# Performance work log

Measured on AMD Instinct MI355X. Metric: run time of the kernel, lower is better.

## Reference

```python
import jax, jax.numpy as jnp
import numpy as np

N = 2048
HID = 1024
Z = 256
DIM = 128 + 64 * 3 + 32 * 5  # 480
FAN = 128 * 128 + 64 * 64 + 32 * 32  # total fan-in over all CG paths


def _ln(x, g, b, eps=1e-6):
    mu = jnp.mean(x, axis=-1, keepdims=True)
    var = jnp.mean((x - mu) ** 2, axis=-1, keepdims=True)
    return (x - mu) * jax.lax.rsqrt(var + eps) * g + b


def _fctp(t, w0, w1, w2):
    # FullyConnectedTensorProduct(irreps, irreps, 'HIDx0e'):
    # only l1==l2 -> 0e paths survive; CG is delta_{m1,m2}/sqrt(2l+1).
    x0 = t[:, :128]                       # 128x0e
    x1 = t[:, 128:320].reshape(-1, 64, 3)  # 64x1o
    x2 = t[:, 320:480].reshape(-1, 32, 5)  # 32x2e
    e0 = jnp.einsum('bu,bv,uvh->bh', x0, x0, w0)
    e1 = jnp.einsum('bum,bvm,uvh->bh', x1, x1, w1) / np.sqrt(3.0)
    e2 = jnp.einsum('bum,bvm,uvh->bh', x2, x2, w2) / np.sqrt(5.0)
    return (e0 + e1 + e2) / np.sqrt(float(FAN))  # component normalization


def _head(t, w0, w1, w2, W1, b1, g1, be1, W2, b2, g2, be2):
    h = _fctp(t, w0, w1, w2)
    h = jax.nn.silu(_ln(h @ W1 + b1, g1, be1))
    h = jax.nn.silu(_ln(h @ W2 + b2, g2, be2))
    return h  # [N, Z]


def setup_inputs() -> dict:
    key = jax.random.key(0)
    ks = jax.random.split(key, 6)
    return {
        'tensor_in': jax.random.normal(ks[0], (N, DIM), jnp.float32),
        'w0': jax.random.normal(ks[1], (128, 128, HID), jnp.float32),
        'w1': jax.random.normal(ks[2], (64, 64, HID), jnp.float32),
        'w2': jax.random.normal(ks[3], (32, 32, HID), jnp.float32),
        'W1': jax.random.normal(ks[4], (HID, HID), jnp.float32) / np.sqrt(HID),
        'b1': jnp.zeros((HID,), jnp.float32),
        'g1': jnp.ones((HID,), jnp.float32),
        'be1': jnp.zeros((HID,), jnp.float32),
        'W2': jax.random.normal(ks[5], (HID, Z), jnp.float32) / np.sqrt(HID),
        'b2': jnp.zeros((Z,), jnp.float32),
        'g2': jnp.ones((Z,), jnp.float32),
        'be2': jnp.zeros((Z,), jnp.float32),
    }


def reference(tensor_in, w0, w1, w2, W1, b1, g1, be1, W2, b2, g2, be2):
    f = lambda t: _head(t, w0, w1, w2, W1, b1, g1, be1, W2, b2, g2, be2)
    x, pullback = jax.vjp(f, tensor_in)
    # torch: grad(x, tensor_in, grad_outputs=ones_like(x), create_graph=True)
    y = pullback(jnp.ones_like(x))[0]
    return x, y
```

## Files before the change

kernel.cpp:

```cpp
#include <hip/hip_runtime.h>
#include <math.h>

typedef unsigned short u16;
typedef __bf16 bf16x8 __attribute__((ext_vector_type(8)));
typedef float f32x4 __attribute__((ext_vector_type(4)));

#define NPACK  11264
#define NVALID 10864
#define BASE1  8256
#define BASE2  10336

__device__ __forceinline__ u16 f2bf(float f) {
    unsigned u = __builtin_bit_cast(unsigned, f);
    u += 0x7FFFu + ((u >> 16) & 1u);
    return (u16)(u >> 16);
}
__device__ __forceinline__ float bf2f(u16 h) {
    return __builtin_bit_cast(float, ((unsigned)h) << 16);
}

#define GLOAD_LDS16(g, l)                                                     \
    __builtin_amdgcn_global_load_lds(                                         \
        (const __attribute__((address_space(1))) void*)(g),                   \
        (__attribute__((address_space(3))) void*)(l), 16, 0, 0)

__device__ __forceinline__ int pk0(int a, int b) {
    int u = min(a, b), v = max(a, b);
    return u * 128 - (u * (u - 1)) / 2 + (v - u);
}
__device__ __forceinline__ int pk1(int a, int b) {
    int u = min(a, b), v = max(a, b);
    return BASE1 + u * 64 - (u * (u - 1)) / 2 + (v - u);
}
__device__ __forceinline__ int pk2(int a, int b) {
    int u = min(a, b), v = max(a, b);
    return BASE2 + u * 32 - (u * (u - 1)) / 2 + (v - u);
}

__global__ __launch_bounds__(256) void k_uvall(u16* __restrict__ tab) {
    int j = blockIdx.x * 256 + threadIdx.x;
    if (j < 16384) {
        int u = j >> 7, v = j & 127;
        if (v >= u) tab[pk0(u, v)] = (u16)((u << 7) | v);
    } else if (j < 20480) {
        int k = j - 16384, u = k >> 6, v = k & 63;
        if (v >= u) tab[pk1(u, v)] = (u16)((1 << 14) | (u << 7) | v);
    } else if (j < 21504) {
        int k = j - 20480, u = k >> 5, v = k & 31;
        if (v >= u) tab[pk2(u, v)] = (u16)((2 << 14) | (u << 7) | v);
    } else {
        int k = j - 21504;
        if (NVALID + k < NPACK) tab[NVALID + k] = 0xFFFFu;
    }
}

__global__ __launch_bounds__(256) void k_packw(const float* __restrict__ w0,
                                               const float* __restrict__ w1,
                                               const float* __restrict__ w2,
                                               const u16* __restrict__ tab,
                                               u16* __restrict__ Wsym,
                                               u16* __restrict__ Wt) {
    __shared__ u16 tile[32][258];
    __shared__ u16 te[32];
    int i0 = blockIdx.x * 32, h0 = blockIdx.y * 256, tid = threadIdx.x;
    if (tid < 32) te[tid] = tab[i0 + tid];
    __syncthreads();
    const float s1 = 0.57735026918962576f, s2 = 0.44721359549995794f;
    for (int il = 0; il < 32; il++) {
        unsigned e = te[il];
        float val = 0.f;
        if ((e >> 14) != 3) {
            int seg = e >> 14, u = (e >> 7) & 127, v = e & 127;
            const float* wb; int S; float sc;
            if (seg == 0)      { wb = w0; S = 128; sc = 1.f; }
            else if (seg == 1) { wb = w1; S = 64;  sc = s1; }
            else               { wb = w2; S = 32;  sc = s2; }
            val = sc * (wb[(size_t)(u * S + v) * 1024 + h0 + tid] +
                        wb[(size_t)(v * S + u) * 1024 + h0 + tid]);
        }
        u16 bv = f2bf(val);
        Wsym[(size_t)(i0 + il) * 1024 + h0 + tid] = bv;
        tile[il][tid] = bv;
    }
    __syncthreads();
    union { u16 a[32]; uint4 q[4]; } pk;
#pragma unroll
    for (int il = 0; il < 32; il++) pk.a[il] = tile[il][tid];
    uint4* dst = (uint4*)(Wt + (size_t)(h0 + tid) * NPACK + i0);
#pragma unroll
    for (int q = 0; q < 4; q++) dst[q] = pk.q[q];
}

__global__ __launch_bounds__(256) void k_convert(const float* __restrict__ in,
                                                 u16* __restrict__ out, int n4) {
    int i = blockIdx.x * 256 + threadIdx.x;
    if (i >= n4) return;
    float4 v = ((const float4*)in)[i];
    union { u16 a[4]; unsigned long long q; } o;
    o.a[0] = f2bf(v.x); o.a[1] = f2bf(v.y); o.a[2] = f2bf(v.z); o.a[3] = f2bf(v.w);
    ((unsigned long long*)out)[i] = o.q;
}

__global__ __launch_bounds__(256) void k_transpose(const float* __restrict__ in, int R, int C,
                                                   u16* __restrict__ out, int ldOut) {
    __shared__ float tile[32][33];
    int tr0 = blockIdx.y * 32;
    int tc0 = blockIdx.x * 32;
    int lr = threadIdx.x >> 5;
    int lc = threadIdx.x & 31;
#pragma unroll
    for (int i = 0; i < 4; i++) {
        int rr = lr + i * 8;
        tile[rr][lc] = in[(size_t)(tr0 + rr) * C + tc0 + lc];
    }
    __syncthreads();
#pragma unroll
    for (int i = 0; i < 4; i++) {
        int rr = lr + i * 8;
        out[(size_t)(tc0 + rr) * ldOut + tr0 + lc] = f2bf(tile[lc][rr]);
    }
}

__global__ __launch_bounds__(256) void k_features_pack(const float* __restrict__ t,
                                                       const u16* __restrict__ tab,
                                                       u16* __restrict__ P) {
    __shared__ u16 tab_s[NPACK];
    __shared__ float tr[480];
    int b = blockIdx.x, tid = threadIdx.x;
    for (int j = tid; j < NPACK / 8; j += 256)
        ((uint4*)tab_s)[j] = ((const uint4*)tab)[j];
    for (int j = tid; j < 480; j += 256) tr[j] = t[(size_t)b * 480 + j];
    __syncthreads();
    u16* row = P + (size_t)b * NPACK;
    for (int i = tid; i < NPACK; i += 256) {
        unsigned e = tab_s[i];
        float p = 0.f;
        if ((e >> 14) != 3) {
            int seg = e >> 14, u = (e >> 7) & 127, v = e & 127;
            if (seg == 0) p = tr[u] * tr[v];
            else if (seg == 1) {
                const float* x1 = tr + 128;
                p = x1[u*3]*x1[v*3] + x1[u*3+1]*x1[v*3+1] + x1[u*3+2]*x1[v*3+2];
            } else {
                const float* x2 = tr + 320;
#pragma unroll
                for (int m = 0; m < 5; m++) p += x2[u*5+m] * x2[v*5+m];
            }
            if (u == v) p *= 0.5f;
        }
        row[i] = f2bf(p);
    }
}

__global__ __launch_bounds__(256) void k_gemm2(const u16* __restrict__ A, int ldA,
                                               const u16* __restrict__ B, int ldB,
                                               int kLen, float scale,
                                               const float* __restrict__ bias,
                                               float* __restrict__ Cf,
                                               u16* __restrict__ Cb, int ldC,
                                               float* __restrict__ Cpart, int Mtot,
                                               int swz) {
    __shared__ u16 As[2][128 * 32];
    __shared__ u16 Bs[2][128 * 32];
    const int tid = threadIdx.x;
    const int wave = tid >> 6, lane = tid & 63;
    const int wm = wave >> 1, wn = wave & 1;
    int nT, mT, z;
    if (swz == 1) {
        int L = blockIdx.x;
        z = L & 7; int r = L >> 3;
        nT = r >> 4; mT = r & 15;
    } else if (swz == 2) {
        int L = blockIdx.x;
        int c = L & 7, r = L >> 3;
        nT = (r % 11) * 8 + c; mT = r / 11; z = 0;
    } else {
        nT = blockIdx.x; mT = blockIdx.y; z = blockIdx.z;
    }
    const int m0 = mT * 128, n0 = nT * 128;
    const size_t kOff = (size_t)z * kLen;

    const int chl = (((lane & 3) ^ ((lane >> 3) & 3))) * 8;
    const u16* aG = A + (size_t)(m0 + wave * 32 + (lane >> 2)) * ldA + kOff + chl;
    const u16* bG = B + (size_t)(n0 + wave * 32 + (lane >> 2)) * ldB + kOff + chl;
    const size_t aS = (size_t)16 * ldA;
    const size_t bS = (size_t)16 * ldB;
    u16* aL0 = &As[0][(wave * 32) * 32];
    u16* aL1 = &As[0][(wave * 32 + 16) * 32];
    u16* aH0 = &As[1][(wave * 32) * 32];
    u16* aH1 = &As[1][(wave * 32 + 16) * 32];
    u16* bL0 = &Bs[0][(wave * 32) * 32];
    u16* bL1 = &Bs[0][(wave * 32 + 16) * 32];
    u16* bH0 = &Bs[1][(wave * 32) * 32];
    u16* bH1 = &Bs[1][(wave * 32 + 16) * 32];

    f32x4 acc[4][4];
#pragma unroll
    for (int i = 0; i < 4; i++)
#pragma unroll
        for (int j = 0; j < 4; j++) acc[i][j] = (f32x4){0.f, 0.f, 0.f, 0.f};

    const int ml = lane & 15, kq8 = lane >> 4;
    const int kqs = (kq8 ^ ((ml >> 1) & 3)) * 8;
    const u16* aRd0 = &As[0][(wm * 64 + ml) * 32 + kqs];
    const u16* bRd0 = &Bs[0][(wn * 64 + ml) * 32 + kqs];
    const u16* aRd1 = &As[1][(wm * 64 + ml) * 32 + kqs];
    const u16* bRd1 = &Bs[1][(wn * 64 + ml) * 32 + kqs];

    for (int k = 0; k < kLen; k += 64) {
        GLOAD_LDS16(aG, aL0);
        GLOAD_LDS16(aG + aS, aL1);
        GLOAD_LDS16(aG + 32, aH0);
        GLOAD_LDS16(aG + aS + 32, aH1);
        GLOAD_LDS16(bG, bL0);
        GLOAD_LDS16(bG + bS, bL1);
        GLOAD_LDS16(bG + 32, bH0);
        GLOAD_LDS16(bG + bS + 32, bH1);
        aG += 64; bG += 64;
        __syncthreads();
        {
            bf16x8 af[4], bfv[4];
#pragma unroll
            for (int i = 0; i < 4; i++) af[i]  = *(const bf16x8*)(aRd0 + i * 16 * 32);
#pragma unroll
            for (int j = 0; j < 4; j++) bfv[j] = *(const bf16x8*)(bRd0 + j * 16 * 32);
#pragma unroll
            for (int i = 0; i < 4; i++)
#pragma unroll
                for (int j = 0; j < 4; j++)
                    acc[i][j] = __builtin_amdgcn_mfma_f32_16x16x32_bf16(af[i], bfv[j], acc[i][j], 0, 0, 0);
        }
        {
            bf16x8 af[4], bfv[4];
#pragma unroll
            for (int i = 0; i < 4; i++) af[i]  = *(const bf16x8*)(aRd1 + i * 16 * 32);
#pragma unroll
            for (int j = 0; j < 4; j++) bfv[j] = *(const bf16x8*)(bRd1 + j * 16 * 32);
#pragma unroll
            for (int i = 0; i < 4; i++)
#pragma unroll
                for (int j = 0; j < 4; j++)
                    acc[i][j] = __builtin_amdgcn_mfma_f32_16x16x32_bf16(af[i], bfv[j], acc[i][j], 0, 0, 0);
        }
        __syncthreads();
    }

    const int q = lane >> 4, nl = lane & 15;
    if (Cpart) {
        float* outP = Cpart + (size_t)z * Mtot * ldC;
#pragma unroll
        for (int i = 0; i < 4; i++)
#pragma unroll
            for (int j = 0; j < 4; j++)
#pragma unroll
                for (int reg = 0; reg < 4; reg++) {
                    int row = m0 + wm * 64 + i * 16 + q * 4 + reg;
                    int col = n0 + wn * 64 + j * 16 + nl;
                    outP[(size_t)row * ldC + col] = acc[i][j][reg];
                }
    } else {
#pragma unroll
        for (int i = 0; i < 4; i++)
#pragma unroll
            for (int j = 0; j < 4; j++)
#pragma unroll
                for (int reg = 0; reg < 4; reg++) {
                    int row = m0 + wm * 64 + i * 16 + q * 4 + reg;
                    int col = n0 + wn * 64 + j * 16 + nl;
                    float v = acc[i][j][reg] * scale + (bias ? bias[col] : 0.0f);
                    if (Cf) Cf[(size_t)row * ldC + col] = v;
                    else    Cb[(size_t)row * ldC + col] = f2bf(v);
                }
    }
}

#define VMCNT0 asm volatile("s_waitcnt vmcnt(0)" ::: "memory")
#define BARX() __builtin_amdgcn_s_barrier()

#define STG_A(p, kh, rh, kb) GLOAD_LDS16(aB + (size_t)(rh) * aH + (kb) + (kh) * 32, \
                                         &As[p][kh][((rh) * 128 + wave * 16) * 32])
#define STG_B(p, kh, rh, kb) GLOAD_LDS16(bB + (size_t)(rh) * bH + (kb) + (kh) * 32, \
                                         &Bs[p][kh][((rh) * 128 + wave * 16) * 32])
#define MMQ(fb, gb, bv) do { _Pragma("unroll") \
    for (int ff = 0; ff < 4; ff++) { _Pragma("unroll") \
        for (int gg = 0; gg < 2; gg++) { \
            acc[(fb)+ff][(gb)+gg] = __builtin_amdgcn_mfma_f32_16x16x32_bf16(a[2*ff],   bv[2*gg],   acc[(fb)+ff][(gb)+gg], 0, 0, 0); \
            acc[(fb)+ff][(gb)+gg] = __builtin_amdgcn_mfma_f32_16x16x32_bf16(a[2*ff+1], bv[2*gg+1], acc[(fb)+ff][(gb)+gg], 0, 0, 0); } } } while (0)

__global__ __launch_bounds__(512, 2) void k_gemm256(const u16* __restrict__ A, int ldA,
                                                    const u16* __restrict__ B, int ldB,
                                                    int kLen, float scale,
                                                    const float* __restrict__ bias,
                                                    u16* __restrict__ Cb, int ldC,
                                                    float* __restrict__ Cpart, int Mtot,
                                                    int swz) {
    __shared__ __align__(16) u16 As[2][2][256 * 32];
    __shared__ __align__(16) u16 Bs[2][2][256 * 32];
    const int tid = threadIdx.x;
    const int lane = tid & 63, wave = tid >> 6;
    const int wm = wave >> 2, wn = wave & 3;
    int mT, nT, z;
    if (swz == 1) {
        z = blockIdx.x & 7; int r = blockIdx.x >> 3; nT = r & 3; mT = r >> 2;
    } else {
        int x = blockIdx.x & 7, j = blockIdx.x >> 3;
        int nti = j >> 3; mT = j & 7;
        if (nti < 5)      nT = nti * 8 + x;
        else if (x < 4)   nT = 40 + x;
        else            { nT = 40 + (x - 4); mT = (j & 7) + 4; }
        z = 0;
    }
    const int m0 = mT * 256, n0 = nT * 256;
    const size_t kOff = (size_t)z * kLen;
    const int nTi = kLen >> 6;

    const int chl = ((tid & 3) ^ ((tid >> 3) & 3)) * 8;
    const u16* aB = A + (size_t)(m0 + (tid >> 2)) * ldA + kOff + chl;
    const u16* bB = B + (size_t)(n0 + (tid >> 2)) * ldB + kOff + chl;
    const size_t aH = (size_t)128 * ldA;
    const size_t bH = (size_t)128 * ldB;

    const int ml = lane & 15, kq8 = lane >> 4;
    const int kqs = (kq8 ^ ((ml >> 1) & 3)) * 8;
    const int aro = (wm * 128 + ml) * 32 + kqs;
    const int bro = (wn * 64 + ml) * 32 + kqs;

    f32x4 acc[8][4];
#pragma unroll
    for (int f = 0; f < 8; f++)
#pragma unroll
        for (int g = 0; g < 4; g++) acc[f][g] = (f32x4){0.f, 0.f, 0.f, 0.f};
    bf16x8 a[8], b[4], b2[4];

    STG_A(0, 0, 0, 0); STG_A(0, 0, 1, 0); STG_A(0, 1, 0, 0); STG_A(0, 1, 1, 0);
    STG_B(0, 0, 0, 0); STG_B(0, 0, 1, 0); STG_B(0, 1, 0, 0); STG_B(0, 1, 1, 0);
    VMCNT0;
    BARX();

    for (int t = 0; t < nTi; t++) {
        const int p = t & 1, p1 = p ^ 1;
        const int kb1 = (t + 1) << 6;
        const bool s1 = (t + 1) < nTi;
#pragma unroll
        for (int f = 0; f < 4; f++) {
            a[2*f]   = *(const bf16x8*)&As[p][0][aro + f * 512];
            a[2*f+1] = *(const bf16x8*)&As[p][1][aro + f * 512];
        }
#pragma unroll
        for (int g = 0; g < 2; g++) {
            b[2*g]   = *(const bf16x8*)&Bs[p][0][bro + g * 512];
            b[2*g+1] = *(const bf16x8*)&Bs[p][1][bro + g * 512];
        }
        if (s1) { STG_A(p1, 0, 0, kb1); STG_A(p1, 0, 1, kb1); }
        BARX();
        __builtin_amdgcn_s_setprio(1);
        MMQ(0, 0, b);
        __builtin_amdgcn_s_setprio(0);
        BARX();
#pragma unroll
        for (int g = 0; g < 2; g++) {
            b2[2*g]   = *(const bf16x8*)&Bs[p][0][bro + (g + 2) * 512];
            b2[2*g+1] = *(const bf16x8*)&Bs[p][1][bro + (g + 2) * 512];
        }
        if (s1) { STG_A(p1, 1, 0, kb1); STG_A(p1, 1, 1, kb1); }
        BARX();
        __builtin_amdgcn_s_setprio(1);
        MMQ(0, 2, b2);
        __builtin_amdgcn_s_setprio(0);
        BARX();
#pragma unroll
        for (int f = 0; f < 4; f++) {
            a[2*f]   = *(const bf16x8*)&As[p][0][aro + (f + 4) * 512];
            a[2*f+1] = *(const bf16x8*)&As[p][1][aro + (f + 4) * 512];
        }
        if (s1) { STG_B(p1, 0, 0, kb1); STG_B(p1, 0, 1, kb1); }
        BARX();
        __builtin_amdgcn_s_setprio(1);
        MMQ(4, 0, b);
        __builtin_amdgcn_s_setprio(0);
        BARX();
        if (s1) { STG_B(p1, 1, 0, kb1); STG_B(p1, 1, 1, kb1); }
        __builtin_amdgcn_s_setprio(1);
        MMQ(4, 2, b2);
        __builtin_amdgcn_s_setprio(0);
        if (s1) VMCNT0;
        BARX();
    }

    const int q = lane >> 4, nl = lane & 15;
    if (Cpart) {
        float* outP = Cpart + (size_t)z * Mtot * ldC;
#pragma unroll
        for (int f = 0; f < 8; f++)
#pragma unroll
            for (int g = 0; g < 4; g++)
#pragma unroll
                for (int reg = 0; reg < 4; reg++) {
                    int row = m0 + wm * 128 + f * 16 + q * 4 + reg;
                    int col = n0 + wn * 64 + g * 16 + nl;
                    outP[(size_t)row * ldC + col] = acc[f][g][reg];
                }
    } else {
#pragma unroll
        for (int f = 0; f < 8; f++)
#pragma unroll
            for (int g = 0; g < 4; g++)
#pragma unroll
                for (int reg = 0; reg < 4; reg++) {
                    int row = m0 + wm * 128 + f * 16 + q * 4 + reg;
                    int col = n0 + wn * 64 + g * 16 + nl;
                    float v = acc[f][g][reg] * scale + (bias ? bias[col] : 0.0f);
                    Cb[(size_t)row * ldC + col] = f2bf(v);
                }
    }
}

__global__ __launch_bounds__(256) void k_reduce(const float* __restrict__ part, size_t stride,
                                                int SK, int total, int N, float scale,
                                                const float* __restrict__ bias,
                                                float* __restrict__ outF, u16* __restrict__ outB) {
    int i = blockIdx.x * 256 + threadIdx.x;
    if (i >= total) return;
    float s = 0.f;
    for (int z = 0; z < SK; z++) s += part[(size_t)z * stride + i];
    float v = s * scale + (bias ? bias[i % N] : 0.0f);
    if (outF) outF[i] = v;
    else      outB[i] = f2bf(v);
}

__device__ __forceinline__ float blockReduce(float v, float* red) {
#pragma unroll
    for (int off = 32; off > 0; off >>= 1) v += __shfl_down(v, off);
    __syncthreads();
    if ((threadIdx.x & 63) == 0) red[threadIdx.x >> 6] = v;
    __syncthreads();
    return red[0] + red[1] + red[2] + red[3];
}

__global__ __launch_bounds__(256) void k_ln_fwd(const float* __restrict__ X, int D,
    const float* __restrict__ g, const float* __restrict__ be,
    float* __restrict__ mu_out, float* __restrict__ r_out,
    u16* __restrict__ a_bf, float* __restrict__ a_f32) {
    __shared__ float red[4];
    int b = blockIdx.x, tid = threadIdx.x;
    const float* x = X + (size_t)b * D;
    int nd = D >> 8;
    float s = 0.f, s2 = 0.f;
    for (int r = 0; r < nd; r++) { float v = x[tid + (r << 8)]; s += v; s2 += v * v; }
    s = blockReduce(s, red);
    s2 = blockReduce(s2, red);
    float mu = s / D;
    float var = s2 / D - mu * mu;
    float rst = rsqrtf(var + 1e-6f);
    if (tid == 0) { mu_out[b] = mu; r_out[b] = rst; }
    for (int r = 0; r < nd; r++) {
        int i = tid + (r << 8);
        float xh = (x[i] - mu) * rst;
        float ln = xh * g[i] + be[i];
        float a = ln / (1.0f + expf(-ln));
        if (a_bf)  a_bf[(size_t)b * D + i] = f2bf(a);
        if (a_f32) a_f32[(size_t)b * D + i] = a;
    }
}

__global__ __launch_bounds__(256) void k_ln_bwd(const float* __restrict__ dup,
    const float* __restrict__ X, const float* __restrict__ mu_in, const float* __restrict__ r_in,
    const float* __restrict__ g, const float* __restrict__ be,
    u16* __restrict__ out_bf, int D) {
    __shared__ float red[4];
    int b = blockIdx.x, tid = threadIdx.x;
    const float* x = X + (size_t)b * D;
    float mu = mu_in[b], rst = r_in[b];
    int nd = D >> 8;
    float w_[4], xh_[4];
    float sw = 0.f, swx = 0.f;
    for (int r = 0; r < nd; r++) {
        int i = tid + (r << 8);
        float xh = (x[i] - mu) * rst;
        float ln = xh * g[i] + be[i];
        float sg = 1.0f / (1.0f + expf(-ln));
        float dsilu = sg * (1.0f + ln * (1.0f - sg));
        float d = dup ? dup[(size_t)b * D + i] : 1.0f;
        float w = g[i] * dsilu * d;
        w_[r] = w; xh_[r] = xh;
        sw += w; swx += w * xh;
    }
    sw = blockReduce(sw, red);
    swx = blockReduce(swx, red);
    float invD = 1.0f / D;
    for (int r = 0; r < nd; r++) {
        int i = tid + (r << 8);
        float dx = rst * (w_[r] - sw * invD - xh_[r] * swx * invD);
        out_bf[(size_t)b * D + i] = f2bf(dx);
    }
}

__global__ __launch_bounds__(256) void k_contract_p(const u16* __restrict__ Gp,
                                                    const float* __restrict__ t,
                                                    float* __restrict__ y) {
    __shared__ u16 gp_s[NPACK];
    __shared__ float xs[480];
    int b = blockIdx.x, tid = threadIdx.x;
    const uint4* gsrc = (const uint4*)(Gp + (size_t)b * NPACK);
    for (int j = tid; j < NPACK / 8; j += 256) ((uint4*)gp_s)[j] = gsrc[j];
    for (int j = tid; j < 480; j += 256) xs[j] = t[(size_t)b * 480 + j];
    __syncthreads();
    int wave = tid >> 6, lane = tid & 63;
    float* yr = y + (size_t)b * 480;
    for (int r = 0; r < 32; r++) {
        int u = wave * 32 + r;
        int v0 = lane, v1 = lane + 64;
        float s = bf2f(gp_s[pk0(u, v0)]) * xs[v0] + bf2f(gp_s[pk0(u, v1)]) * xs[v1];
#pragma unroll
        for (int off = 32; off > 0; off >>= 1) s += __shfl_down(s, off);
        if (lane == 0) yr[u] = s;
    }
    for (int r = 0; r < 16; r++) {
        int u = wave * 16 + r;
        float gv = bf2f(gp_s[pk1(u, lane)]);
        float a0 = gv * xs[128 + lane * 3 + 0];
        float a1 = gv * xs[128 + lane * 3 + 1];
        float a2 = gv * xs[128 + lane * 3 + 2];
#pragma unroll
        for (int off = 32; off > 0; off >>= 1) {
            a0 += __shfl_down(a0, off);
            a1 += __shfl_down(a1, off);
            a2 += __shfl_down(a2, off);
        }
        if (lane == 0) {
            yr[128 + u * 3 + 0] = a0;
            yr[128 + u * 3 + 1] = a1;
            yr[128 + u * 3 + 2] = a2;
        }
    }
    for (int r = 0; r < 8; r++) {
        int u = wave * 8 + r;
        bool act = lane < 32;
        float gv = act ? bf2f(gp_s[pk2(u, act ? lane : 0)]) : 0.f;
        float a[5];
#pragma unroll
        for (int m = 0; m < 5; m++)
            a[m] = act ? gv * xs[320 + lane * 5 + m] : 0.f;
#pragma unroll
        for (int off = 32; off > 0; off >>= 1)
#pragma unroll
            for (int m = 0; m < 5; m++) a[m] += __shfl_down(a[m], off);
        if (lane == 0)
#pragma unroll
            for (int m = 0; m < 5; m++) yr[320 + u * 5 + m] = a[m];
    }
}

extern "C" void kernel_launch(void* const* d_in, const int* in_sizes, int n_in,
                              void* d_out, int out_size, void* d_ws, size_t ws_size,
                              hipStream_t stream) {
    const float* t   = (const float*)d_in[0];
    const float* w0  = (const float*)d_in[1];
    const float* w1  = (const float*)d_in[2];
    const float* w2  = (const float*)d_in[3];
    const float* W1  = (const float*)d_in[4];
    const float* b1  = (const float*)d_in[5];
    const float* g1  = (const float*)d_in[6];
    const float* be1 = (const float*)d_in[7];
    const float* W2  = (const float*)d_in[8];
    const float* b2  = (const float*)d_in[9];
    const float* g2  = (const float*)d_in[10];
    const float* be2 = (const float*)d_in[11];

    float* xout = (float*)d_out;
    float* yout = xout + (size_t)2048 * 256;

    char* ws = (char*)d_ws;
    size_t off = 0;
    auto alloc = [&](size_t bytes) -> void* {
        void* p = ws + off;
        off += (bytes + 255) & ~(size_t)255;
        return p;
    };
    u16*   PG    = (u16*)alloc((size_t)2048 * NPACK * 2);
    u16*   Wsym  = (u16*)alloc((size_t)NPACK * 1024 * 2);
    u16*   Wt    = (u16*)alloc((size_t)1024 * NPACK * 2);
    u16*   uvtab = (u16*)alloc((size_t)NPACK * 2);
    u16*   W1b   = (u16*)alloc((size_t)1024 * 1024 * 2);
    u16*   W1tb  = (u16*)alloc((size_t)1024 * 1024 * 2);
    u16*   W2b   = (u16*)alloc((size_t)1024 * 256 * 2);
    u16*   W2tb  = (u16*)alloc((size_t)256 * 1024 * 2);
    u16*   h_bf  = (u16*)alloc((size_t)2048 * 1024 * 2);
    float* h1pre = (float*)alloc((size_t)2048 * 1024 * 4);
    float* mu1   = (float*)alloc(2048 * 4);
    float* r1    = (float*)alloc(2048 * 4);
    u16*   a1_bf = (u16*)alloc((size_t)2048 * 1024 * 2);
    float* h2pre = (float*)alloc((size_t)2048 * 256 * 4);
    float* mu2   = (float*)alloc(2048 * 4);
    float* r2    = (float*)alloc(2048 * 4);
    u16*   dh2b  = (u16*)alloc((size_t)2048 * 256 * 2);
    float* d_a1  = (float*)alloc((size_t)2048 * 1024 * 4);
    u16*   dh1b  = (u16*)alloc((size_t)2048 * 1024 * 2);
    u16*   de_bf = (u16*)alloc((size_t)2048 * 1024 * 2);
    float* Cpart = (float*)(ws + off);
    size_t cpartBytes = (ws_size > off) ? (ws_size - off) : 0;
    (void)in_sizes; (void)n_in; (void)out_size;

    const float sF = 1.0f / sqrtf(21504.0f);

    auto gemm = [&](const u16* A, int ldA, const u16* B, int ldB, int M, int N, int K,
                    int SKwant, float scale, const float* bias,
                    float* Cf, u16* Cb, int ldC) {
        int SK = SKwant;
        size_t slice = (size_t)M * ldC * 4;
        if (SK > 1 && cpartBytes < 2 * slice) SK = 1;
        if (SK > 1 && (size_t)SK * slice > cpartBytes) SK = (int)(cpartBytes / slice);
        while (SK > 1 && !((K % SK) == 0 && ((K / SK) % 64) == 0)) SK--;
        dim3 grid(N / 128, M / 128, SK);
        if (SK > 1) {
            k_gemm2<<<grid, 256, 0, stream>>>(A, ldA, B, ldB, K / SK, 0.f, nullptr,
                                              nullptr, nullptr, ldC, Cpart, M, 0);
            int total = M * ldC;
            k_reduce<<<(total + 255) / 256, 256, 0, stream>>>(Cpart, (size_t)M * ldC, SK,
                                                              total, N, scale, bias, Cf, Cb);
        } else {
            k_gemm2<<<grid, 256, 0, stream>>>(A, ldA, B, ldB, K, scale, bias,
                                              Cf, Cb, ldC, nullptr, M, 0);
        }
    };

    k_uvall<<<(21504 + NPACK - NVALID + 255) / 256, 256, 0, stream>>>(uvtab);
    k_packw<<<dim3(NPACK / 32, 4), 256, 0, stream>>>(w0, w1, w2, uvtab, Wsym, Wt);

    k_transpose<<<dim3(32, 32), 256, 0, stream>>>(W1, 1024, 1024, W1tb, 1024);
    k_transpose<<<dim3(8, 32), 256, 0, stream>>>(W2, 1024, 256, W2tb, 1024);
    k_convert<<<1024 * 1024 / 1024, 256, 0, stream>>>(W1, W1b, 1024 * 1024 / 4);
    k_convert<<<1024 * 256 / 1024, 256, 0, stream>>>(W2, W2b, 1024 * 256 / 4);

    k_features_pack<<<2048, 256, 0, stream>>>(t, uvtab, PG);

    k_gemm256<<<dim3(256), 512, 0, stream>>>(PG, NPACK, Wt, NPACK, NPACK / 8, 0.f, nullptr,
                                             nullptr, 1024, Cpart, 2048, 1);
    {
        int total = 2048 * 1024;
        k_reduce<<<(total + 255) / 256, 256, 0, stream>>>(Cpart, (size_t)2048 * 1024, 8,
                                                          total, 1024, sF, nullptr,
                                                          nullptr, h_bf);
    }

    gemm(h_bf, 1024, W1tb, 1024, 2048, 1024, 1024, 4, 1.0f, b1, h1pre, nullptr, 1024);
    k_ln_fwd<<<2048, 256, 0, stream>>>(h1pre, 1024, g1, be1, mu1, r1, a1_bf, nullptr);
    gemm(a1_bf, 1024, W2tb, 1024, 2048, 256, 1024, 8, 1.0f, b2, h2pre, nullptr, 256);
    k_ln_fwd<<<2048, 256, 0, stream>>>(h2pre, 256, g2, be2, mu2, r2, nullptr, xout);

    k_ln_bwd<<<2048, 256, 0, stream>>>(nullptr, h2pre, mu2, r2, g2, be2, dh2b, 256);
    gemm(dh2b, 256, W2b, 256, 2048, 1024, 256, 4, 1.0f, nullptr, d_a1, nullptr, 1024);
    k_ln_bwd<<<2048, 256, 0, stream>>>(d_a1, h1pre, mu1, r1, g1, be1, dh1b, 1024);
    gemm(dh1b, 1024, W1b, 1024, 2048, 1024, 1024, 4, sF, nullptr, nullptr, de_bf, 1024);

    u16* Gp = PG;
    k_gemm256<<<dim3(352), 512, 0, stream>>>(de_bf, 1024, Wsym, 1024, 1024, 1.0f, nullptr,
                                             Gp, NPACK, nullptr, 2048, 2);

    k_contract_p<<<2048, 256, 0, stream>>>(Gp, t, yout);
}
```

Baseline: 515.7 us.

## Simplify 256-tile GEMM main loop: issue all prefetches up front, drop inner barriers

Restructures the k_gemm256 main loop so that all eight global-to-LDS prefetches for the next K tile are issued at the start of the iteration. All B fragments are loaded into one register array, and the four MFMA quadrants run back-to-back without intermediate barriers or setprio toggling. The aim is to cut barrier and sync overhead and give the scheduler a longer uninterrupted MFMA stream. The cost is higher register pressure from the larger B array, and the loss of the interleaved ping-pong scheduling that kept waves staggered between memory and matrix work.

```diff
diff --git a/kernel.cpp b/kernel.cpp
--- a/kernel.cpp
+++ b/kernel.cpp
@@ -281,11 +281,11 @@
                                          &As[p][kh][((rh) * 128 + wave * 16) * 32])
 #define STG_B(p, kh, rh, kb) GLOAD_LDS16(bB + (size_t)(rh) * bH + (kb) + (kh) * 32, \
                                          &Bs[p][kh][((rh) * 128 + wave * 16) * 32])
-#define MMQ(fb, gb, bv) do { _Pragma("unroll") \
+#define MMQ2(fb, gb) do { _Pragma("unroll") \
     for (int ff = 0; ff < 4; ff++) { _Pragma("unroll") \
         for (int gg = 0; gg < 2; gg++) { \
-            acc[(fb)+ff][(gb)+gg] = __builtin_amdgcn_mfma_f32_16x16x32_bf16(a[2*ff],   bv[2*gg],   acc[(fb)+ff][(gb)+gg], 0, 0, 0); \
-            acc[(fb)+ff][(gb)+gg] = __builtin_amdgcn_mfma_f32_16x16x32_bf16(a[2*ff+1], bv[2*gg+1], acc[(fb)+ff][(gb)+gg], 0, 0, 0); } } } while (0)
+            acc[(fb)+ff][(gb)+gg] = __builtin_amdgcn_mfma_f32_16x16x32_bf16(a[2*ff],   b[2*((gb)+gg)],   acc[(fb)+ff][(gb)+gg], 0, 0, 0); \
+            acc[(fb)+ff][(gb)+gg] = __builtin_amdgcn_mfma_f32_16x16x32_bf16(a[2*ff+1], b[2*((gb)+gg)+1], acc[(fb)+ff][(gb)+gg], 0, 0, 0); } } } while (0)
 
 __global__ __launch_bounds__(512, 2) void k_gemm256(const u16* __restrict__ A, int ldA,
                                                     const u16* __restrict__ B, int ldB,
@@ -330,7 +330,7 @@
     for (int f = 0; f < 8; f++)
 #pragma unroll
         for (int g = 0; g < 4; g++) acc[f][g] = (f32x4){0.f, 0.f, 0.f, 0.f};
-    bf16x8 a[8], b[4], b2[4];
+    bf16x8 a[8], b[8];
 
     STG_A(0, 0, 0, 0); STG_A(0, 0, 1, 0); STG_A(0, 1, 0, 0); STG_A(0, 1, 1, 0);
     STG_B(0, 0, 0, 0); STG_B(0, 0, 1, 0); STG_B(0, 1, 0, 0); STG_B(0, 1, 1, 0);
@@ -341,48 +341,31 @@
         const int p = t & 1, p1 = p ^ 1;
         const int kb1 = (t + 1) << 6;
         const bool s1 = (t + 1) < nTi;
+        if (s1) {
+            STG_A(p1, 0, 0, kb1); STG_A(p1, 0, 1, kb1);
+            STG_A(p1, 1, 0, kb1); STG_A(p1, 1, 1, kb1);
+            STG_B(p1, 0, 0, kb1); STG_B(p1, 0, 1, kb1);
+            STG_B(p1, 1, 0, kb1); STG_B(p1, 1, 1, kb1);
+        }
 #pragma unroll
         for (int f = 0; f < 4; f++) {
             a[2*f]   = *(const bf16x8*)&As[p][0][aro + f * 512];
             a[2*f+1] = *(const bf16x8*)&As[p][1][aro + f * 512];
         }
 #pragma unroll
-        for (int g = 0; g < 2; g++) {
+        for (int g = 0; g < 4; g++) {
             b[2*g]   = *(const bf16x8*)&Bs[p][0][bro + g * 512];
             b[2*g+1] = *(const bf16x8*)&Bs[p][1][bro + g * 512];
         }
-        if (s1) { STG_A(p1, 0, 0, kb1); STG_A(p1, 0, 1, kb1); }
-        BARX();
-        __builtin_amdgcn_s_setprio(1);
-        MMQ(0, 0, b);
-        __builtin_amdgcn_s_setprio(0);
-        BARX();
-#pragma unroll
-        for (int g = 0; g < 2; g++) {
-            b2[2*g]   = *(const bf16x8*)&Bs[p][0][bro + (g + 2) * 512];
-            b2[2*g+1] = *(const bf16x8*)&Bs[p][1][bro + (g + 2) * 512];
-        }
-        if (s1) { STG_A(p1, 1, 0, kb1); STG_A(p1, 1, 1, kb1); }
-        BARX();
-        __builtin_amdgcn_s_setprio(1);
-        MMQ(0, 2, b2);
-        __builtin_amdgcn_s_setprio(0);
-        BARX();
+        MMQ2(0, 0);
+        MMQ2(0, 2);
 #pragma unroll
         for (int f = 0; f < 4; f++) {
             a[2*f]   = *(const bf16x8*)&As[p][0][aro + (f + 4) * 512];
             a[2*f+1] = *(const bf16x8*)&As[p][1][aro + (f + 4) * 512];
         }
-        if (s1) { STG_B(p1, 0, 0, kb1); STG_B(p1, 0, 1, kb1); }
-        BARX();
-        __builtin_amdgcn_s_setprio(1);
-        MMQ(4, 0, b);
-        __builtin_amdgcn_s_setprio(0);
-        BARX();
-        if (s1) { STG_B(p1, 1, 0, kb1); STG_B(p1, 1, 1, kb1); }
-        __builtin_amdgcn_s_setprio(1);
-        MMQ(4, 2, b2);
-        __builtin_amdgcn_s_setprio(0);
+        MMQ2(4, 0);
+        MMQ2(4, 2);
         if (s1) VMCNT0;
         BARX();
     }
```

Result: slower. 540.8 us (+4.9%).
